# Performance work log

Measured on AMD Instinct MI355X. Metric: run time of the kernel, lower is better.

## Reference

```python
import jax, jax.numpy as jnp
import numpy as np

# Config constants (match init_kwargs)
E = 32          # num_experts
K = 4           # num_experts_per_token
G = 4           # num_expert_group
TG = 2          # topk_group
H = 2048        # hidden_size
F = 1024        # moe_intermediate_size
FS = 2048       # shared expert intermediate (moe_intermediate_size * num_shared_experts)
SCALE = 2.0     # routed_scaling_factor
B, S = 2, 1024
N = B * S
CAP = 2 * (N * K // E)


def setup_inputs() -> dict:
    key = jax.random.key(0)
    ks = jax.random.split(key, 9)
    w = 0.02  # init scale for weights
    return {
        "hidden_states": jax.random.normal(ks[0], (B, S, H), jnp.float32),
        "gate_w": jax.random.normal(ks[1], (E, H), jnp.float32) * w,
        "gate_bias": jax.random.normal(ks[2], (E,), jnp.float32) * w,
        "w1": jax.random.normal(ks[3], (E, H, F), jnp.float32) * w,
        "w2": jax.random.normal(ks[4], (E, F, H), jnp.float32) * w,
        "w3": jax.random.normal(ks[5], (E, H, F), jnp.float32) * w,
        "shared_gate": jax.random.normal(ks[6], (H, FS), jnp.float32) * w,
        "shared_up": jax.random.normal(ks[7], (H, FS), jnp.float32) * w,
        "shared_down": jax.random.normal(ks[8], (FS, H), jnp.float32) * w,
    }


def _gate(x, gate_w, gate_bias):
    # x: [N, H] -> (topk_idx [N,K] int32, topk_w [N,K] f32)
    logits = x @ gate_w.T                       # [N, E]
    scores = jax.nn.sigmoid(logits)
    sc = scores + gate_bias                     # scores_for_choice
    n = x.shape[0]
    grp = sc.reshape(n, G, E // G)
    group_scores = jax.lax.top_k(grp, 2)[0].sum(-1)          # [N, G]
    _, gidx = jax.lax.top_k(group_scores, TG)                # [N, TG]
    gmask = jnp.zeros((n, G), sc.dtype).at[jnp.arange(n)[:, None], gidx].set(1.0)
    smask = jnp.repeat(gmask, E // G, axis=1)                # [N, E]
    tmp = jnp.where(smask > 0, sc, 0.0)
    _, topk_idx = jax.lax.top_k(tmp, K)                      # [N, K]
    topk_w = jnp.take_along_axis(scores, topk_idx, axis=1)
    topk_w = topk_w / (topk_w.sum(-1, keepdims=True) + 1e-20)  # renormalize (K>1)
    return topk_idx, topk_w * SCALE


def _moe(x, topk_idx, topk_w, w1, w2, w3):
    # Capacity-based dispatch -> grouped SwiGLU GEMMs -> weighted combine.
    n = x.shape[0]
    flat_e = topk_idx.reshape(-1)                            # [N*K]
    oh = jax.nn.one_hot(flat_e, E, dtype=jnp.int32)
    pos = (jnp.cumsum(oh, axis=0) * oh).sum(-1) - 1          # slot within expert
    keep = pos < CAP
    slot = jnp.where(keep, pos, CAP)                         # CAP -> dropped via mode='drop'
    x_rep = jnp.repeat(x, K, axis=0)                         # [N*K, H]
    buf = jnp.zeros((E, CAP, H), x.dtype).at[flat_e, slot].set(x_rep, mode='drop')
    h = jax.nn.silu(jnp.einsum('ech,ehf->ecf', buf, w1)) * jnp.einsum('ech,ehf->ecf', buf, w3)
    ob = jnp.einsum('ecf,efh->ech', h, w2)                   # [E, CAP, H]
    y = ob[flat_e, jnp.minimum(slot, CAP - 1)]               # [N*K, H]
    y = jnp.where(keep[:, None], y, 0.0)
    return (y.reshape(n, K, H) * topk_w[:, :, None]).sum(1)  # [N, H]


def reference(hidden_states, gate_w, gate_bias, w1, w2, w3, shared_gate, shared_up, shared_down):
    b, s, h = hidden_states.shape
    x = hidden_states.reshape(-1, h)
    topk_idx, topk_w = _gate(x, gate_w, gate_bias)
    out = _moe(x, topk_idx, topk_w, w1, w2, w3)
    shared = (jax.nn.silu(x @ shared_gate) * (x @ shared_up)) @ shared_down
    return (out + shared).reshape(b, s, h)
```

## Files before the change

### kernel.cpp

```cpp
#include <hip/hip_runtime.h>
#include <stdint.h>
#include <math.h>

#define NTOK 2048
#define HDIM 2048
#define FDIM 1024
#define NEXP 32
#define TOPK 4
#define NGRP 4
#define CAP  512

typedef _Float16 f16;
typedef _Float16 half8 __attribute__((ext_vector_type(8)));
typedef float f32x4 __attribute__((ext_vector_type(4)));

__device__ __forceinline__ int swz3(int n) { return (n ^ (n >> 2)) & 3; }

__global__ __launch_bounds__(256) void convert_kernel(const float* __restrict__ x,
                                                      f16* __restrict__ xbt) {
  int i = blockIdx.x * 256 + threadIdx.x;
  int r = i >> 8;
  int c8 = (i & 255) << 3;
  const float* p = x + (size_t)r * HDIM + c8;
  f32x4 a = *(const f32x4*)p;
  f32x4 b = *(const f32x4*)(p + 4);
  half8 v;
  v[0] = (f16)a[0]; v[1] = (f16)a[1]; v[2] = (f16)a[2]; v[3] = (f16)a[3];
  v[4] = (f16)b[0]; v[5] = (f16)b[1]; v[6] = (f16)b[2]; v[7] = (f16)b[3];
  int t = c8 >> 5;
  *(half8*)((char*)xbt + (size_t)t * 131072 + r * 64 + (c8 & 31) * 2) = v;
}

__global__ __launch_bounds__(256) void gate_kernel(const float* __restrict__ x,
                                                   const float* __restrict__ gw,
                                                   const float* __restrict__ gb,
                                                   int* __restrict__ tidx,
                                                   float* __restrict__ tw) {
  int t = blockIdx.x;
  int tid = threadIdx.x;
  int e = tid >> 3, p = tid & 7;
  const f32x4* xr = (const f32x4*)(x + (size_t)t * HDIM);
  const f32x4* wr = (const f32x4*)(gw + (size_t)e * HDIM);
  float s = 0.f;
  for (int c = 0; c < 64; c++) {
    f32x4 a = xr[p + c * 8], w = wr[p + c * 8];
    s += a[0] * w[0] + a[1] * w[1] + a[2] * w[2] + a[3] * w[3];
  }
  s += __shfl_down(s, 4, 8);
  s += __shfl_down(s, 2, 8);
  s += __shfl_down(s, 1, 8);
  __shared__ float lg[NEXP];
  if (p == 0) lg[e] = s;
  __syncthreads();
  if (tid == 0) {
    float sc[NEXP], scb[NEXP];
    for (int i = 0; i < NEXP; i++) {
      sc[i] = 1.f / (1.f + expf(-lg[i]));
      scb[i] = sc[i] + gb[i];
    }
    float gs[NGRP];
    for (int g = 0; g < NGRP; g++) {
      float m1 = -1e30f, m2 = -1e30f;
      for (int j = 0; j < 8; j++) {
        float v = scb[g * 8 + j];
        if (v > m1) { m2 = m1; m1 = v; }
        else if (v > m2) m2 = v;
      }
      gs[g] = m1 + m2;
    }
    int g1 = 0; float bv = gs[0];
    for (int g = 1; g < NGRP; g++) if (gs[g] > bv) { bv = gs[g]; g1 = g; }
    int g2 = -1; bv = -1e30f;
    for (int g = 0; g < NGRP; g++) if (g != g1 && gs[g] > bv) { bv = gs[g]; g2 = g; }
    float cand[NEXP];
    for (int i = 0; i < NEXP; i++) {
      int g = i >> 3;
      cand[i] = (g == g1 || g == g2) ? scb[i] : 0.0f;
    }
    int isel[TOPK]; float wsel[TOPK]; float wsum = 0.f;
    bool used[NEXP] = {};
    for (int k = 0; k < TOPK; k++) {
      int best = 0; float bw = -1e30f;
      for (int i = 0; i < NEXP; i++)
        if (!used[i] && cand[i] > bw) { bw = cand[i]; best = i; }
      used[best] = true;
      isel[k] = best;
      wsel[k] = sc[best];
      wsum += wsel[k];
    }
    float inv = 2.0f / (wsum + 1e-20f);
    for (int k = 0; k < TOPK; k++) {
      tidx[t * TOPK + k] = isel[k];
      tw[t * TOPK + k] = wsel[k] * inv;
    }
  }
}

__global__ __launch_bounds__(256) void dispatch_kernel(const int* __restrict__ tidx,
                                                       const float* __restrict__ tw,
                                                       int* __restrict__ tok,
                                                       float* __restrict__ wt,
                                                       int* __restrict__ cnt) {
  int e = blockIdx.x, tid = threadIdx.x, wv = tid >> 6, lane = tid & 63;
  __shared__ int wsum[4];
  __shared__ int sbase;
  if (tid == 0) sbase = 0;
  __syncthreads();
  for (int c = 0; c < (NTOK * TOPK) / 256; c++) {
    int i = c * 256 + tid;
    int fe = tidx[i];
    bool flag = (fe == e);
    unsigned long long b = __ballot(flag ? 1 : 0);
    int lr = __popcll(b & ((1ull << lane) - 1ull));
    if (lane == 0) wsum[wv] = __popcll(b);
    __syncthreads();
    int off = 0;
    for (int w2 = 0; w2 < wv; w2++) off += wsum[w2];
    int tot = wsum[0] + wsum[1] + wsum[2] + wsum[3];
    int base = sbase;
    if (flag) {
      int pos = base + off + lr;
      if (pos < CAP) {
        tok[e * CAP + pos] = i >> 2;
        wt[e * CAP + pos] = tw[i];
      }
    }
    __syncthreads();
    if (tid == 0) sbase = base + tot;
  }
  __syncthreads();
  if (tid == 0) cnt[e] = min(sbase, CAP);
}

__global__ __launch_bounds__(256) void gather_kernel(const f16* __restrict__ xbt,
                                                     const int* __restrict__ tok,
                                                     const int* __restrict__ cnt,
                                                     f16* __restrict__ xg) {
  int bid = blockIdx.x;
  int t = bid & 63, e = bid >> 6;
  int cn = cnt[e];
  int tid = threadIdx.x;
  char* dst = (char*)xg + (size_t)e * 2097152 + (size_t)t * 32768;
  const char* srcb = (const char*)xbt + (size_t)t * 131072;
  for (int s = tid; s < cn; s += 256) {
    const uint4* sp = (const uint4*)(srcb + (size_t)tok[e * CAP + s] * 64);
    uint4 v0 = sp[0], v1 = sp[1], v2 = sp[2], v3 = sp[3];
    uint4* dp = (uint4*)(dst + s * 64);
    dp[0] = v0; dp[1] = v1; dp[2] = v2; dp[3] = v3;
  }
}

template<int MODE>
__global__ __launch_bounds__(256, 2)
void gemm_kernel(const f16* __restrict__ Ag, const float* __restrict__ B0g,
                 const float* __restrict__ B1g, void* __restrict__ outp,
                 const int* __restrict__ tokL, const float* __restrict__ wtL,
                 const int* __restrict__ cntP) {
  constexpr bool ROUTED = (MODE == 0 || MODE == 2);
  constexpr bool DUAL = (MODE <= 1);
  constexpr bool WIDE = (MODE == 2);
  constexpr bool SINGLE = (MODE == 3);
  constexpr int MF = ROUTED ? 6 : 4;
  constexpr int WM = MF * 16;
  constexpr int BM = WM * 4;
  constexpr int KD = (MODE == 2) ? 1024 : 2048;
  constexpr int NK = KD / 32;
  constexpr int ND = (MODE == 0) ? 1024 : 2048;
  constexpr size_t TS = ROUTED ? 32768 : 131072;
  constexpr int LDSB = (SINGLE ? 1 : 2) * 2048;

  int bid = blockIdx.x;
  int tid = threadIdx.x, lane = tid & 63, wv = tid >> 6;

  int e = 0, mstart = 0, n0;
  if constexpr (ROUTED) {
    int x = bid & 7, j = bid >> 3;
    e = x + 8 * (j >> 5);
    n0 = (j & 31) * ((MODE == 0) ? 32 : 64);
  } else {
    mstart = (bid & 7) * 256;
    n0 = (bid >> 3) * 32;
  }

  const char* Ab = (const char*)Ag;
  const float* B0 = B0g;
  const float* B1 = B1g;
  int Mcur = NTOK;
  if constexpr (ROUTED) {
    Mcur = cntP[e];
    Ab += (size_t)e * ((MODE == 0) ? 2097152 : 1048576);
    B0 += (size_t)e * ((size_t)KD * ND);
    if constexpr (DUAL) B1 += (size_t)e * ((size_t)KD * ND);
  }

  __shared__ __align__(16) char lds[2 * LDSB];

  int kb = tid >> 3;
  int nb4 = (tid & 7) * 4;
  const float* Bk0 = B0 + (size_t)kb * ND + n0 + nb4;
  const float* Bk1 = DUAL ? (B1 + (size_t)kb * ND + n0 + nb4) : nullptr;

  f32x4 sA0, sA1, sB0, sB1, sC0, sC1, sD0, sD1;
  half8 af[MF];
  half8 bf0[2];
  half8 bf1[SINGLE ? 1 : 2];

#define LOADB(tt, X0, X1) { \
    const float* _p = Bk0 + (size_t)(tt) * (32 * ND); \
    X0 = *(const f32x4*)_p; \
    if constexpr (DUAL) X1 = *(const f32x4*)(Bk1 + (size_t)(tt) * (32 * ND)); \
    else if constexpr (WIDE) X1 = *(const f32x4*)(_p + 32); }

#define WRITEB(X0, X1, par) { \
    char* _b = lds + (par) * LDSB; \
    _Pragma("unroll") \
    for (int _q = 0; _q < 4; _q++) { \
      int _n = nb4 + _q; \
      int _off = _n * 64 + (((kb >> 3) ^ swz3(_n)) << 4) + (kb & 7) * 2; \
      *(f16*)(_b + _off) = (f16)X0[_q]; \
      if constexpr (!SINGLE) *(f16*)(_b + 2048 + _off) = (f16)X1[_q]; \
    } }

#define BFREAD(par) { \
    _Pragma("unroll") \
    for (int _f = 0; _f < 2; _f++) { \
      int _n = _f * 16 + (lane & 15); \
      int _off = (par) * LDSB + _n * 64 + (((lane >> 4) ^ swz3(_n)) << 4); \
      bf0[_f] = *(const half8*)(lds + _off); \
      if constexpr (!SINGLE) bf1[_f] = *(const half8*)(lds + 2048 + _off); \
    } }

#define LOADA(tt) { \
    _Pragma("unroll") \
    for (int _m = 0; _m < MF; _m++) \
      af[_m] = *(const half8*)(Ab + (size_t)(tt) * TS + aoff[_m]); }

#define DOMFMA() { \
    _Pragma("unroll") \
    for (int _m = 0; _m < MF; _m++) { \
      _Pragma("unroll") \
      for (int _f = 0; _f < 2; _f++) { \
        acc0[_m][_f] = __builtin_amdgcn_mfma_f32_16x16x32_f16(af[_m], bf0[_f], acc0[_m][_f], 0, 0, 0); \
        if constexpr (!SINGLE) \
          acc1[_m][_f] = __builtin_amdgcn_mfma_f32_16x16x32_f16(af[_m], bf1[_f], acc1[_m][_f], 0, 0, 0); \
      } } }

#define SYNC() { asm volatile("s_waitcnt lgkmcnt(0)" ::: "memory"); __builtin_amdgcn_s_barrier(); }

  int m0 = mstart;
  while (true) {
    unsigned aoff[MF];
#pragma unroll
    for (int mf = 0; mf < MF; mf++) {
      int row = m0 + wv * WM + mf * 16 + (lane & 15);
      aoff[mf] = row * 64 + ((lane >> 4) << 4);
    }

    f32x4 acc0[MF][2];
    f32x4 acc1[SINGLE ? 1 : MF][SINGLE ? 1 : 2];
#pragma unroll
    for (int mf = 0; mf < MF; mf++)
#pragma unroll
      for (int f = 0; f < 2; f++) acc0[mf][f] = (f32x4){0.f, 0.f, 0.f, 0.f};
    if constexpr (!SINGLE) {
#pragma unroll
      for (int mf = 0; mf < MF; mf++)
#pragma unroll
        for (int f = 0; f < 2; f++) acc1[mf][f] = (f32x4){0.f, 0.f, 0.f, 0.f};
    }

    LOADB(0, sA0, sA1)
    LOADB(1, sB0, sB1)
    LOADB(2, sC0, sC1)
    LOADB(3, sD0, sD1)
    WRITEB(sA0, sA1, 0)
    LOADA(0)
    SYNC()

    for (int u = 0; u < NK; u += 4) {
      BFREAD(0)
      WRITEB(sB0, sB1, 1)
      if (u + 4 < NK) LOADB(u + 4, sA0, sA1)
      DOMFMA()
      LOADA(u + 1)
      SYNC()
      BFREAD(1)
      WRITEB(sC0, sC1, 0)
      if (u + 5 < NK) LOADB(u + 5, sB0, sB1)
      DOMFMA()
      LOADA(u + 2)
      SYNC()
      BFREAD(0)
      WRITEB(sD0, sD1, 1)
      if (u + 6 < NK) LOADB(u + 6, sC0, sC1)
      DOMFMA()
      LOADA(u + 3)
      SYNC()
      BFREAD(1)
      if (u + 4 < NK) WRITEB(sA0, sA1, 0)
      if (u + 7 < NK) LOADB(u + 7, sD0, sD1)
      DOMFMA()
      if (u + 4 < NK) {
        LOADA(u + 4)
        SYNC()
      }
    }

    int koff = (lane >> 4) << 2;
    if constexpr (MODE == 0) {
      char* Hb = (char*)outp + (size_t)e * 1048576;
#pragma unroll
      for (int mf = 0; mf < MF; mf++)
#pragma unroll
        for (int j = 0; j < 4; j++) {
          int slot = m0 + wv * WM + mf * 16 + koff + j;
          if (slot < Mcur) {
#pragma unroll
            for (int f = 0; f < 2; f++) {
              int col = n0 + f * 16 + (lane & 15);
              float g = acc0[mf][f][j], u = acc1[mf][f][j];
              float val = g / (1.f + expf(-g)) * u;
              *(f16*)(Hb + (size_t)(col >> 5) * 32768 + slot * 64 + (col & 31) * 2) = (f16)val;
            }
          }
        }
    } else if constexpr (MODE == 1) {
      char* Hb = (char*)outp;
#pragma unroll
      for (int mf = 0; mf < MF; mf++)
#pragma unroll
        for (int j = 0; j < 4; j++) {
          int row = m0 + wv * WM + mf * 16 + koff + j;
#pragma unroll
          for (int f = 0; f < 2; f++) {
            int col = n0 + f * 16 + (lane & 15);
            float g = acc0[mf][f][j], u = acc1[mf][f][j];
            float val = g / (1.f + expf(-g)) * u;
            *(f16*)(Hb + (size_t)(col >> 5) * 131072 + row * 64 + (col & 31) * 2) = (f16)val;
          }
        }
    } else if constexpr (MODE == 2) {
      float* Of = (float*)outp;
      const int* tokp = tokL + e * CAP;
      const float* wtp = wtL + e * CAP;
#pragma unroll
      for (int mf = 0; mf < MF; mf++)
#pragma unroll
        for (int j = 0; j < 4; j++) {
          int slot = m0 + wv * WM + mf * 16 + koff + j;
          if (slot < Mcur) {
            int tk = tokp[slot];
            float w = wtp[slot];
#pragma unroll
            for (int f = 0; f < 2; f++) {
              int col = n0 + f * 16 + (lane & 15);
              atomicAdd(Of + (size_t)tk * HDIM + col, acc0[mf][f][j] * w);
              atomicAdd(Of + (size_t)tk * HDIM + col + 32, acc1[mf][f][j] * w);
            }
          }
        }
    } else {
      float* Of = (float*)outp;
#pragma unroll
      for (int mf = 0; mf < MF; mf++)
#pragma unroll
        for (int j = 0; j < 4; j++) {
          int row = m0 + wv * WM + mf * 16 + koff + j;
#pragma unroll
          for (int f = 0; f < 2; f++) {
            int col = n0 + f * 16 + (lane & 15);
            Of[(size_t)row * HDIM + col] = acc0[mf][f][j];
          }
        }
    }

    m0 += BM;
    if (!(ROUTED && m0 < Mcur)) break;
  }

#undef LOADB
#undef WRITEB
#undef BFREAD
#undef LOADA
#undef DOMFMA
#undef SYNC
}

extern "C" void kernel_launch(void* const* d_in, const int* in_sizes, int n_in,
                              void* d_out, int out_size, void* d_ws, size_t ws_size,
                              hipStream_t stream) {
  const float* x  = (const float*)d_in[0];
  const float* gw = (const float*)d_in[1];
  const float* gb = (const float*)d_in[2];
  const float* w1 = (const float*)d_in[3];
  const float* w2 = (const float*)d_in[4];
  const float* w3 = (const float*)d_in[5];
  const float* sg = (const float*)d_in[6];
  const float* su = (const float*)d_in[7];
  const float* sd = (const float*)d_in[8];
  float* out = (float*)d_out;
  char* ws = (char*)d_ws;

  f16*   xbt = (f16*)(ws);
  f16*   hs  = (f16*)(ws + 8388608);
  f16*   hbuf= (f16*)(ws + 16777216);
  f16*   xg  = (f16*)(ws + 50331648);
  int*   tok = (int*)(ws + 117440512);
  float* wt  = (float*)(ws + 117506048);
  int*   tidx= (int*)(ws + 117571584);
  float* tw  = (float*)(ws + 117604352);
  int*   cnt = (int*)(ws + 117637120);

  convert_kernel<<<2048, 256, 0, stream>>>(x, xbt);
  gate_kernel<<<2048, 256, 0, stream>>>(x, gw, gb, tidx, tw);
  dispatch_kernel<<<32, 256, 0, stream>>>(tidx, tw, tok, wt, cnt);
  gather_kernel<<<2048, 256, 0, stream>>>(xbt, tok, cnt, xg);

  gemm_kernel<0><<<1024, 256, 0, stream>>>(xg, w1, w3, hbuf, tok, wt, cnt);
  gemm_kernel<1><<<512, 256, 0, stream>>>(xbt, sg, su, hs, nullptr, nullptr, nullptr);
  gemm_kernel<3><<<512, 256, 0, stream>>>(hs, sd, nullptr, out, nullptr, nullptr, nullptr);
  gemm_kernel<2><<<1024, 256, 0, stream>>>(hbuf, w2, nullptr, out, tok, wt, cnt);
}
```

Measured before the change: 604.3 us.

## Fuse convert into gate kernel and retile routed GEMMs with fixed M tiles

Merges the fp32-to-fp16 conversion into the gate kernel so x is read once and one launch is saved. The routed expert GEMMs move to a new 2-wave kernel with 256-row tiles, at most two M tiles per expert, and early exit when the tile is past the expert's count. This replaces the per-expert loop over M. The new kernel loads two K rows per thread, writes packed half2 values to LDS, and uses a 2-stage B pipeline. Each wave holds more accumulators, which may raise register pressure.

```diff
diff --git a/kernel.cpp b/kernel.cpp
--- a/kernel.cpp
+++ b/kernel.cpp
@@ -12,30 +12,17 @@
 
 typedef _Float16 f16;
 typedef _Float16 half8 __attribute__((ext_vector_type(8)));
+typedef _Float16 half2v __attribute__((ext_vector_type(2)));
 typedef float f32x4 __attribute__((ext_vector_type(4)));
 
 __device__ __forceinline__ int swz3(int n) { return (n ^ (n >> 2)) & 3; }
 
-__global__ __launch_bounds__(256) void convert_kernel(const float* __restrict__ x,
-                                                      f16* __restrict__ xbt) {
-  int i = blockIdx.x * 256 + threadIdx.x;
-  int r = i >> 8;
-  int c8 = (i & 255) << 3;
-  const float* p = x + (size_t)r * HDIM + c8;
-  f32x4 a = *(const f32x4*)p;
-  f32x4 b = *(const f32x4*)(p + 4);
-  half8 v;
-  v[0] = (f16)a[0]; v[1] = (f16)a[1]; v[2] = (f16)a[2]; v[3] = (f16)a[3];
-  v[4] = (f16)b[0]; v[5] = (f16)b[1]; v[6] = (f16)b[2]; v[7] = (f16)b[3];
-  int t = c8 >> 5;
-  *(half8*)((char*)xbt + (size_t)t * 131072 + r * 64 + (c8 & 31) * 2) = v;
-}
-
-__global__ __launch_bounds__(256) void gate_kernel(const float* __restrict__ x,
-                                                   const float* __restrict__ gw,
-                                                   const float* __restrict__ gb,
-                                                   int* __restrict__ tidx,
-                                                   float* __restrict__ tw) {
+__global__ __launch_bounds__(256) void gateconv_kernel(const float* __restrict__ x,
+                                                       const float* __restrict__ gw,
+                                                       const float* __restrict__ gb,
+                                                       int* __restrict__ tidx,
+                                                       float* __restrict__ tw,
+                                                       f16* __restrict__ xbt) {
   int t = blockIdx.x;
   int tid = threadIdx.x;
   int e = tid >> 3, p = tid & 7;
@@ -51,6 +38,18 @@
   s += __shfl_down(s, 1, 8);
   __shared__ float lg[NEXP];
   if (p == 0) lg[e] = s;
+
+  {
+    int c8 = tid * 8;
+    const float* pp = x + (size_t)t * HDIM + c8;
+    f32x4 a = *(const f32x4*)pp;
+    f32x4 b = *(const f32x4*)(pp + 4);
+    half8 v;
+    v[0] = (f16)a[0]; v[1] = (f16)a[1]; v[2] = (f16)a[2]; v[3] = (f16)a[3];
+    v[4] = (f16)b[0]; v[5] = (f16)b[1]; v[6] = (f16)b[2]; v[7] = (f16)b[3];
+    *(half8*)((char*)xbt + (size_t)(c8 >> 5) * 131072 + t * 64 + (c8 & 31) * 2) = v;
+  }
+
   __syncthreads();
   if (tid == 0) {
     float sc[NEXP], scb[NEXP];
@@ -151,47 +150,198 @@
 }
 
 template<int MODE>
+__global__ __launch_bounds__(128, 2)
+void gemm2_kernel(const f16* __restrict__ Ag, const float* __restrict__ B0g,
+                  const float* __restrict__ B1g, void* __restrict__ outp,
+                  const int* __restrict__ tokL, const float* __restrict__ wtL,
+                  const int* __restrict__ cntP) {
+  constexpr bool UP = (MODE == 0);
+  constexpr int KD = UP ? 2048 : 1024;
+  constexpr int NK = KD / 32;
+  constexpr int ND = UP ? 1024 : 2048;
+
+  int bid = blockIdx.x;
+  int e = (bid & 7) + (((bid >> 3) & 3) << 3);
+  int m0 = ((bid >> 5) & 1) * 256;
+  int n0 = (bid >> 6) * (UP ? 32 : 64);
+
+  int cnt_e = cntP[e];
+  if (m0 >= cnt_e) return;
+
+  const char* Ab = (const char*)Ag + (size_t)e * (UP ? 2097152 : 1048576);
+  const float* B0 = B0g + (size_t)e * ((size_t)KD * ND);
+  const float* B1 = UP ? (B1g + (size_t)e * ((size_t)KD * ND)) : nullptr;
+
+  int tid = threadIdx.x, lane = tid & 63, wv = tid >> 6;
+
+  int n4 = (tid & 7) * 4;
+  int kp = (tid >> 3) * 2;
+  const float* Bk0 = B0 + (size_t)kp * ND + n0 + n4;
+  const float* Bk1 = UP ? (B1 + (size_t)kp * ND + n0 + n4)
+                        : (B0 + (size_t)kp * ND + n0 + 32 + n4);
+
+  __shared__ __align__(16) char lds[8192];
+
+  unsigned aoff[8];
+#pragma unroll
+  for (int mf = 0; mf < 8; mf++) {
+    int row = m0 + wv * 128 + mf * 16 + (lane & 15);
+    aoff[mf] = row * 64 + ((lane >> 4) << 4);
+  }
+
+  f32x4 acc0[8][2], acc1[8][2];
+#pragma unroll
+  for (int mf = 0; mf < 8; mf++)
+#pragma unroll
+    for (int f = 0; f < 2; f++) {
+      acc0[mf][f] = (f32x4){0.f, 0.f, 0.f, 0.f};
+      acc1[mf][f] = (f32x4){0.f, 0.f, 0.f, 0.f};
+    }
+
+  half8 af[8];
+  half8 bf0[2], bf1[2];
+  f32x4 E0, E1, E2, E3, O0, O1, O2, O3;
+
+#define LOADB(tt, S0, S1, S2, S3) { \
+    size_t _b = (size_t)(tt) * (32 * ND); \
+    S0 = *(const f32x4*)(Bk0 + _b); \
+    S1 = *(const f32x4*)(Bk0 + _b + ND); \
+    S2 = *(const f32x4*)(Bk1 + _b); \
+    S3 = *(const f32x4*)(Bk1 + _b + ND); }
+
+#define WRITEB(S0, S1, S2, S3, par) { \
+    char* _base = lds + (par) * 4096; \
+    _Pragma("unroll") \
+    for (int _q = 0; _q < 4; _q++) { \
+      int _n = n4 + _q; \
+      int _off = _n * 64 + (((kp >> 3) ^ swz3(_n)) << 4) + (kp & 7) * 2; \
+      half2v _h0; _h0[0] = (f16)S0[_q]; _h0[1] = (f16)S1[_q]; \
+      *(half2v*)(_base + _off) = _h0; \
+      half2v _h1; _h1[0] = (f16)S2[_q]; _h1[1] = (f16)S3[_q]; \
+      *(half2v*)(_base + 2048 + _off) = _h1; \
+    } }
+
+#define BFREAD(par) { \
+    _Pragma("unroll") \
+    for (int _f = 0; _f < 2; _f++) { \
+      int _n = _f * 16 + (lane & 15); \
+      int _off = (par) * 4096 + _n * 64 + (((lane >> 4) ^ swz3(_n)) << 4); \
+      bf0[_f] = *(const half8*)(lds + _off); \
+      bf1[_f] = *(const half8*)(lds + 2048 + _off); \
+    } }
+
+#define LOADA(tt) { \
+    _Pragma("unroll") \
+    for (int _m = 0; _m < 8; _m++) \
+      af[_m] = *(const half8*)(Ab + (size_t)(tt) * 32768 + aoff[_m]); }
+
+#define DOMFMA() { \
+    _Pragma("unroll") \
+    for (int _m = 0; _m < 8; _m++) { \
+      _Pragma("unroll") \
+      for (int _f = 0; _f < 2; _f++) { \
+        acc0[_m][_f] = __builtin_amdgcn_mfma_f32_16x16x32_f16(af[_m], bf0[_f], acc0[_m][_f], 0, 0, 0); \
+        acc1[_m][_f] = __builtin_amdgcn_mfma_f32_16x16x32_f16(af[_m], bf1[_f], acc1[_m][_f], 0, 0, 0); \
+      } } }
+
+#define SYNC() { asm volatile("s_waitcnt lgkmcnt(0)" ::: "memory"); __builtin_amdgcn_s_barrier(); }
+
+  LOADB(0, E0, E1, E2, E3)
+  LOADB(1, O0, O1, O2, O3)
+  WRITEB(E0, E1, E2, E3, 0)
+  LOADA(0)
+  SYNC()
+
+  for (int t = 0; t < NK; t += 2) {
+    BFREAD(0)
+    WRITEB(O0, O1, O2, O3, 1)
+    if (t + 2 < NK) LOADB(t + 2, E0, E1, E2, E3)
+    DOMFMA()
+    LOADA(t + 1)
+    SYNC()
+    BFREAD(1)
+    if (t + 2 < NK) {
+      WRITEB(E0, E1, E2, E3, 0)
+      if (t + 3 < NK) LOADB(t + 3, O0, O1, O2, O3)
+    }
+    DOMFMA()
+    if (t + 2 < NK) {
+      LOADA(t + 2)
+      SYNC()
+    }
+  }
+
+#undef LOADB
+#undef WRITEB
+#undef BFREAD
+#undef LOADA
+#undef DOMFMA
+#undef SYNC
+
+  int koff = (lane >> 4) << 2;
+  if constexpr (MODE == 0) {
+    char* Hb = (char*)outp + (size_t)e * 1048576;
+#pragma unroll
+    for (int mf = 0; mf < 8; mf++)
+#pragma unroll
+      for (int j = 0; j < 4; j++) {
+        int slot = m0 + wv * 128 + mf * 16 + koff + j;
+        if (slot < cnt_e) {
+#pragma unroll
+          for (int f = 0; f < 2; f++) {
+            int col = n0 + f * 16 + (lane & 15);
+            float g = acc0[mf][f][j], u = acc1[mf][f][j];
+            float val = g / (1.f + expf(-g)) * u;
+            *(f16*)(Hb + (size_t)(col >> 5) * 32768 + slot * 64 + (col & 31) * 2) = (f16)val;
+          }
+        }
+      }
+  } else {
+    float* Of = (float*)outp;
+    const int* tokp = tokL + e * CAP;
+    const float* wtp = wtL + e * CAP;
+#pragma unroll
+    for (int mf = 0; mf < 8; mf++)
+#pragma unroll
+      for (int j = 0; j < 4; j++) {
+        int slot = m0 + wv * 128 + mf * 16 + koff + j;
+        if (slot < cnt_e) {
+          int tk = tokp[slot];
+          float w = wtp[slot];
+#pragma unroll
+          for (int f = 0; f < 2; f++) {
+            int col = n0 + f * 16 + (lane & 15);
+            atomicAdd(Of + (size_t)tk * HDIM + col, acc0[mf][f][j] * w);
+            atomicAdd(Of + (size_t)tk * HDIM + col + 32, acc1[mf][f][j] * w);
+          }
+        }
+      }
+  }
+}
+
+template<int MODE>
 __global__ __launch_bounds__(256, 2)
 void gemm_kernel(const f16* __restrict__ Ag, const float* __restrict__ B0g,
-                 const float* __restrict__ B1g, void* __restrict__ outp,
-                 const int* __restrict__ tokL, const float* __restrict__ wtL,
-                 const int* __restrict__ cntP) {
-  constexpr bool ROUTED = (MODE == 0 || MODE == 2);
-  constexpr bool DUAL = (MODE <= 1);
-  constexpr bool WIDE = (MODE == 2);
+                 const float* __restrict__ B1g, void* __restrict__ outp) {
+  constexpr bool DUAL = (MODE == 1);
   constexpr bool SINGLE = (MODE == 3);
-  constexpr int MF = ROUTED ? 6 : 4;
-  constexpr int WM = MF * 16;
-  constexpr int BM = WM * 4;
-  constexpr int KD = (MODE == 2) ? 1024 : 2048;
+  constexpr int MF = 4;
+  constexpr int WM = 64;
+  constexpr int KD = 2048;
   constexpr int NK = KD / 32;
-  constexpr int ND = (MODE == 0) ? 1024 : 2048;
-  constexpr size_t TS = ROUTED ? 32768 : 131072;
+  constexpr int ND = 2048;
+  constexpr size_t TS = 131072;
   constexpr int LDSB = (SINGLE ? 1 : 2) * 2048;
 
   int bid = blockIdx.x;
   int tid = threadIdx.x, lane = tid & 63, wv = tid >> 6;
 
-  int e = 0, mstart = 0, n0;
-  if constexpr (ROUTED) {
-    int x = bid & 7, j = bid >> 3;
-    e = x + 8 * (j >> 5);
-    n0 = (j & 31) * ((MODE == 0) ? 32 : 64);
-  } else {
-    mstart = (bid & 7) * 256;
-    n0 = (bid >> 3) * 32;
-  }
+  int mstart = (bid & 7) * 256;
+  int n0 = (bid >> 3) * 32;
 
   const char* Ab = (const char*)Ag;
   const float* B0 = B0g;
   const float* B1 = B1g;
-  int Mcur = NTOK;
-  if constexpr (ROUTED) {
-    Mcur = cntP[e];
-    Ab += (size_t)e * ((MODE == 0) ? 2097152 : 1048576);
-    B0 += (size_t)e * ((size_t)KD * ND);
-    if constexpr (DUAL) B1 += (size_t)e * ((size_t)KD * ND);
-  }
 
   __shared__ __align__(16) char lds[2 * LDSB];
 
@@ -208,8 +358,7 @@
 #define LOADB(tt, X0, X1) { \
     const float* _p = Bk0 + (size_t)(tt) * (32 * ND); \
     X0 = *(const f32x4*)_p; \
-    if constexpr (DUAL) X1 = *(const f32x4*)(Bk1 + (size_t)(tt) * (32 * ND)); \
-    else if constexpr (WIDE) X1 = *(const f32x4*)(_p + 32); }
+    if constexpr (DUAL) X1 = *(const f32x4*)(Bk1 + (size_t)(tt) * (32 * ND)); }
 
 #define WRITEB(X0, X1, par) { \
     char* _b = lds + (par) * LDSB; \
@@ -248,134 +397,61 @@
 #define SYNC() { asm volatile("s_waitcnt lgkmcnt(0)" ::: "memory"); __builtin_amdgcn_s_barrier(); }
 
   int m0 = mstart;
-  while (true) {
-    unsigned aoff[MF];
-#pragma unroll
-    for (int mf = 0; mf < MF; mf++) {
-      int row = m0 + wv * WM + mf * 16 + (lane & 15);
-      aoff[mf] = row * 64 + ((lane >> 4) << 4);
-    }
-
-    f32x4 acc0[MF][2];
-    f32x4 acc1[SINGLE ? 1 : MF][SINGLE ? 1 : 2];
+  unsigned aoff[MF];
+#pragma unroll
+  for (int mf = 0; mf < MF; mf++) {
+    int row = m0 + wv * WM + mf * 16 + (lane & 15);
+    aoff[mf] = row * 64 + ((lane >> 4) << 4);
+  }
+
+  f32x4 acc0[MF][2];
+  f32x4 acc1[SINGLE ? 1 : MF][SINGLE ? 1 : 2];
+#pragma unroll
+  for (int mf = 0; mf < MF; mf++)
+#pragma unroll
+    for (int f = 0; f < 2; f++) acc0[mf][f] = (f32x4){0.f, 0.f, 0.f, 0.f};
+  if constexpr (!SINGLE) {
 #pragma unroll
     for (int mf = 0; mf < MF; mf++)
 #pragma unroll
-      for (int f = 0; f < 2; f++) acc0[mf][f] = (f32x4){0.f, 0.f, 0.f, 0.f};
-    if constexpr (!SINGLE) {
-#pragma unroll
-      for (int mf = 0; mf < MF; mf++)
-#pragma unroll
-        for (int f = 0; f < 2; f++) acc1[mf][f] = (f32x4){0.f, 0.f, 0.f, 0.f};
-    }
-
-    LOADB(0, sA0, sA1)
-    LOADB(1, sB0, sB1)
-    LOADB(2, sC0, sC1)
-    LOADB(3, sD0, sD1)
-    WRITEB(sA0, sA1, 0)
-    LOADA(0)
+      for (int f = 0; f < 2; f++) acc1[mf][f] = (f32x4){0.f, 0.f, 0.f, 0.f};
+  }
+
+  LOADB(0, sA0, sA1)
+  LOADB(1, sB0, sB1)
+  LOADB(2, sC0, sC1)
+  LOADB(3, sD0, sD1)
+  WRITEB(sA0, sA1, 0)
+  LOADA(0)
+  SYNC()
+
+  for (int u = 0; u < NK; u += 4) {
+    BFREAD(0)
+    WRITEB(sB0, sB1, 1)
+    if (u + 4 < NK) LOADB(u + 4, sA0, sA1)
+    DOMFMA()
+    LOADA(u + 1)
     SYNC()
-
-    for (int u = 0; u < NK; u += 4) {
-      BFREAD(0)
-      WRITEB(sB0, sB1, 1)
-      if (u + 4 < NK) LOADB(u + 4, sA0, sA1)
-      DOMFMA()
-      LOADA(u + 1)
+    BFREAD(1)
+    WRITEB(sC0, sC1, 0)
+    if (u + 5 < NK) LOADB(u + 5, sB0, sB1)
+    DOMFMA()
+    LOADA(u + 2)
+    SYNC()
+    BFREAD(0)
+    WRITEB(sD0, sD1, 1)
+    if (u + 6 < NK) LOADB(u + 6, sC0, sC1)
+    DOMFMA()
+    LOADA(u + 3)
+    SYNC()
+    BFREAD(1)
+    if (u + 4 < NK) WRITEB(sA0, sA1, 0)
+    if (u + 7 < NK) LOADB(u + 7, sD0, sD1)
+    DOMFMA()
+    if (u + 4 < NK) {
+      LOADA(u + 4)
       SYNC()
-      BFREAD(1)
-      WRITEB(sC0, sC1, 0)
-      if (u + 5 < NK) LOADB(u + 5, sB0, sB1)
-      DOMFMA()
-      LOADA(u + 2)
-      SYNC()
-      BFREAD(0)
-      WRITEB(sD0, sD1, 1)
-      if (u + 6 < NK) LOADB(u + 6, sC0, sC1)
-      DOMFMA()
-      LOADA(u + 3)
-      SYNC()
-      BFREAD(1)
-      if (u + 4 < NK) WRITEB(sA0, sA1, 0)
-      if (u + 7 < NK) LOADB(u + 7, sD0, sD1)
-      DOMFMA()
-      if (u + 4 < NK) {
-        LOADA(u + 4)
-        SYNC()
-      }
-    }
-
-    int koff = (lane >> 4) << 2;
-    if constexpr (MODE == 0) {
-      char* Hb = (char*)outp + (size_t)e * 1048576;
-#pragma unroll
-      for (int mf = 0; mf < MF; mf++)
-#pragma unroll
-        for (int j = 0; j < 4; j++) {
-          int slot = m0 + wv * WM + mf * 16 + koff + j;
-          if (slot < Mcur) {
-#pragma unroll
-            for (int f = 0; f < 2; f++) {
-              int col = n0 + f * 16 + (lane & 15);
-              float g = acc0[mf][f][j], u = acc1[mf][f][j];
-              float val = g / (1.f + expf(-g)) * u;
-              *(f16*)(Hb + (size_t)(col >> 5) * 32768 + slot * 64 + (col & 31) * 2) = (f16)val;
-            }
-          }
-        }
-    } else if constexpr (MODE == 1) {
-      char* Hb = (char*)outp;
-#pragma unroll
-      for (int mf = 0; mf < MF; mf++)
-#pragma unroll
-        for (int j = 0; j < 4; j++) {
-          int row = m0 + wv * WM + mf * 16 + koff + j;
-#pragma unroll
-          for (int f = 0; f < 2; f++) {
-            int col = n0 + f * 16 + (lane & 15);
-            float g = acc0[mf][f][j], u = acc1[mf][f][j];
-            float val = g / (1.f + expf(-g)) * u;
-            *(f16*)(Hb + (size_t)(col >> 5) * 131072 + row * 64 + (col & 31) * 2) = (f16)val;
-          }
-        }
-    } else if constexpr (MODE == 2) {
-      float* Of = (float*)outp;
-      const int* tokp = tokL + e * CAP;
-      const float* wtp = wtL + e * CAP;
-#pragma unroll
-      for (int mf = 0; mf < MF; mf++)
-#pragma unroll
-        for (int j = 0; j < 4; j++) {
-          int slot = m0 + wv * WM + mf * 16 + koff + j;
-          if (slot < Mcur) {
-            int tk = tokp[slot];
-            float w = wtp[slot];
-#pragma unroll
-            for (int f = 0; f < 2; f++) {
-              int col = n0 + f * 16 + (lane & 15);
-              atomicAdd(Of + (size_t)tk * HDIM + col, acc0[mf][f][j] * w);
-              atomicAdd(Of + (size_t)tk * HDIM + col + 32, acc1[mf][f][j] * w);
-            }
-          }
-        }
-    } else {
-      float* Of = (float*)outp;
-#pragma unroll
-      for (int mf = 0; mf < MF; mf++)
-#pragma unroll
-        for (int j = 0; j < 4; j++) {
-          int row = m0 + wv * WM + mf * 16 + koff + j;
-#pragma unroll
-          for (int f = 0; f < 2; f++) {
-            int col = n0 + f * 16 + (lane & 15);
-            Of[(size_t)row * HDIM + col] = acc0[mf][f][j];
-          }
-        }
-    }
-
-    m0 += BM;
-    if (!(ROUTED && m0 < Mcur)) break;
+    }
   }
 
 #undef LOADB
@@ -384,6 +460,37 @@
 #undef LOADA
 #undef DOMFMA
 #undef SYNC
+
+  int koff = (lane >> 4) << 2;
+  if constexpr (MODE == 1) {
+    char* Hb = (char*)outp;
+#pragma unroll
+    for (int mf = 0; mf < MF; mf++)
+#pragma unroll
+      for (int j = 0; j < 4; j++) {
+        int row = m0 + wv * WM + mf * 16 + koff + j;
+#pragma unroll
+        for (int f = 0; f < 2; f++) {
+          int col = n0 + f * 16 + (lane & 15);
+          float g = acc0[mf][f][j], u = acc1[mf][f][j];
+          float val = g / (1.f + expf(-g)) * u;
+          *(f16*)(Hb + (size_t)(col >> 5) * 131072 + row * 64 + (col & 31) * 2) = (f16)val;
+        }
+      }
+  } else {
+    float* Of = (float*)outp;
+#pragma unroll
+    for (int mf = 0; mf < MF; mf++)
+#pragma unroll
+      for (int j = 0; j < 4; j++) {
+        int row = m0 + wv * WM + mf * 16 + koff + j;
+#pragma unroll
+        for (int f = 0; f < 2; f++) {
+          int col = n0 + f * 16 + (lane & 15);
+          Of[(size_t)row * HDIM + col] = acc0[mf][f][j];
+        }
+      }
+  }
 }
 
 extern "C" void kernel_launch(void* const* d_in, const int* in_sizes, int n_in,
@@ -411,13 +518,12 @@
   float* tw  = (float*)(ws + 117604352);
   int*   cnt = (int*)(ws + 117637120);
 
-  convert_kernel<<<2048, 256, 0, stream>>>(x, xbt);
-  gate_kernel<<<2048, 256, 0, stream>>>(x, gw, gb, tidx, tw);
+  gateconv_kernel<<<2048, 256, 0, stream>>>(x, gw, gb, tidx, tw, xbt);
   dispatch_kernel<<<32, 256, 0, stream>>>(tidx, tw, tok, wt, cnt);
   gather_kernel<<<2048, 256, 0, stream>>>(xbt, tok, cnt, xg);
 
-  gemm_kernel<0><<<1024, 256, 0, stream>>>(xg, w1, w3, hbuf, tok, wt, cnt);
-  gemm_kernel<1><<<512, 256, 0, stream>>>(xbt, sg, su, hs, nullptr, nullptr, nullptr);
-  gemm_kernel<3><<<512, 256, 0, stream>>>(hs, sd, nullptr, out, nullptr, nullptr, nullptr);
-  gemm_kernel<2><<<1024, 256, 0, stream>>>(hbuf, w2, nullptr, out, tok, wt, cnt);
+  gemm2_kernel<0><<<2048, 128, 0, stream>>>(xg, w1, w3, hbuf, tok, wt, cnt);
+  gemm_kernel<1><<<512, 256, 0, stream>>>(xbt, sg, su, hs);
+  gemm_kernel<3><<<512, 256, 0, stream>>>(hs, sd, nullptr, out);
+  gemm2_kernel<2><<<2048, 128, 0, stream>>>(hbuf, w2, nullptr, out, tok, wt, cnt);
 }
```

New measurement: 598.5 us. No clear change (-1.0%).
